# Optimization experiments

Hardware: AMD Instinct MI355X
Metric: run time of the kernel (lower is better)

Reference implementation:

```python
import jax, jax.numpy as jnp
import numpy as np


def setup_inputs() -> dict:
    key = jax.random.key(0)
    k1, k2 = jax.random.split(key)
    B, Te, Td, D = 16, 1024, 1024, 1024
    encoder_outputs = jax.random.normal(k1, (B, Te, D), dtype=jnp.float32)
    decoder_outputs = jax.random.normal(k2, (B, Td, D), dtype=jnp.float32)
    return {"encoder_outputs": encoder_outputs, "decoder_outputs": decoder_outputs}


def reference(encoder_outputs, decoder_outputs):
    # Luong score: [B, Te, Td] = enc @ dec^T
    luong_score = jnp.einsum("bed,btd->bet", encoder_outputs, decoder_outputs)
    # softmax over encoder-time axis (axis=1), matching K.softmax(..., axis=1)
    attn = jax.nn.softmax(luong_score, axis=1)
    # context vector: sum over encoder time of enc * attn -> [B, Td, D]
    # (original materializes [B, Te, Td, D]; this einsum is the same math)
    encoder_vector = jnp.einsum("bed,bet->btd", encoder_outputs, attn)
    return jnp.concatenate([decoder_outputs, encoder_vector], axis=-1)
```

## Files before the change

kernel.cpp:

```cpp
#include <hip/hip_runtime.h>
#include <hip/hip_bf16.h>
#include <stdint.h>

typedef __bf16 bf16x8 __attribute__((ext_vector_type(8)));
typedef float f32x4 __attribute__((ext_vector_type(4)));

#define B_DIM 16
#define TD 1024
#define TE 1024
#define DD 1024

typedef __attribute__((address_space(1))) void as1_void;
typedef __attribute__((address_space(3))) void as3_void;

#define GLL16(gp, lp) \
  __builtin_amdgcn_global_load_lds((as1_void*)(gp), (as3_void*)(lp), 16, 0, 0)

__device__ __forceinline__ uint32_t rne_bf16(float x) {
  uint32_t u = __builtin_bit_cast(uint32_t, x);
  return (u + 0x7FFFu + ((u >> 16) & 1u)) >> 16;
}

__device__ __forceinline__ void split2(float x, uint32_t& hi, uint32_t& lo) {
  uint32_t h = rne_bf16(x);
  float hf = __builtin_bit_cast(float, h << 16);
  hi = h;
  lo = rne_bf16(x - hf);
}

__global__ __launch_bounds__(256)
void p0a_split_dec(const float4* __restrict__ dec4, uint32_t* __restrict__ dhi,
                   uint32_t* __restrict__ dlo) {
  size_t g = (size_t)blockIdx.x * 256 + threadIdx.x;
#pragma unroll
  for (int s = 0; s < 8; ++s, g += 524288) {
    float4 v = dec4[g];
    uint32_t h0, l0, h1, l1, h2, l2, h3, l3;
    split2(v.x, h0, l0);
    split2(v.y, h1, l1);
    split2(v.z, h2, l2);
    split2(v.w, h3, l3);
    *(uint2*)&dhi[g * 2] = make_uint2(h0 | (h1 << 16), h2 | (h3 << 16));
    *(uint2*)&dlo[g * 2] = make_uint2(l0 | (l1 << 16), l2 | (l3 << 16));
  }
}

__global__ __launch_bounds__(256)
void p0b_split_enc(const float* __restrict__ enc, uint32_t* __restrict__ ehi,
                   uint32_t* __restrict__ elo, uint16_t* __restrict__ eT) {
  __shared__ uint16_t TT[64][65];
  const int tid = threadIdx.x;
  const int b = blockIdx.z;
  const int d0 = (blockIdx.x & 15) * 64, e0 = (blockIdx.x >> 4) * 64;
  const float* src = enc + (size_t)b * TE * DD;
#pragma unroll
  for (int s = 0; s < 4; ++s) {
    int c = tid + 256 * s;
    int row = c >> 4, c4 = c & 15;
    float4 v = *(const float4*)(src + (size_t)(e0 + row) * DD + d0 + c4 * 4);
    uint32_t h0, l0, h1, l1, h2, l2, h3, l3;
    split2(v.x, h0, l0);
    split2(v.y, h1, l1);
    split2(v.z, h2, l2);
    split2(v.w, h3, l3);
    size_t o = (((size_t)b * TE + e0 + row) * DD + d0 + c4 * 4) >> 1;
    *(uint2*)&ehi[o] = make_uint2(h0 | (h1 << 16), h2 | (h3 << 16));
    *(uint2*)&elo[o] = make_uint2(l0 | (l1 << 16), l2 | (l3 << 16));
    TT[row][c4 * 4 + 0] = (uint16_t)h0;
    TT[row][c4 * 4 + 1] = (uint16_t)h1;
    TT[row][c4 * 4 + 2] = (uint16_t)h2;
    TT[row][c4 * 4 + 3] = (uint16_t)h3;
  }
  __syncthreads();
#pragma unroll
  for (int s = 0; s < 4; ++s) {
    int c = tid + 256 * s;
    int d = c >> 4, e4 = c & 15;
    uint32_t w0 = (uint32_t)TT[e4 * 4 + 0][d] | ((uint32_t)TT[e4 * 4 + 1][d] << 16);
    uint32_t w1 = (uint32_t)TT[e4 * 4 + 2][d] | ((uint32_t)TT[e4 * 4 + 3][d] << 16);
    *(uint2*)&eT[((size_t)b * DD + d0 + d) * TE + e0 + e4 * 4] = make_uint2(w0, w1);
  }
}

__global__ __launch_bounds__(256, 2)
void k1_scores_v2(const uint16_t* __restrict__ dhi, const uint16_t* __restrict__ dlo,
                  const uint16_t* __restrict__ ehi, const uint16_t* __restrict__ elo,
                  float* __restrict__ out) {
  __shared__ uint32_t AhU[2048], AlU[2048], BhU[2048], BlU[2048];
  const int tid = threadIdx.x;
  const int lane = tid & 63;
  const int wave = tid >> 6;
  const int wm = wave >> 1, wn = wave & 1;
  const int b = blockIdx.z;
  const int t0 = blockIdx.y * 128, e0 = blockIdx.x * 128;

  const int r2 = tid >> 2, c16 = tid & 3;
  const size_t abase = ((size_t)b * TD + t0 + r2) * DD + c16 * 8;
  const size_t bbase = ((size_t)b * TE + e0 + r2) * DD + c16 * 8;

  const int lr = lane & 15, q = lane >> 4;
  int aoff[4], boff[4];
#pragma unroll
  for (int i = 0; i < 4; ++i) {
    aoff[i] = (wm * 64 + i * 16 + lr) * 16 + q * 4;
    boff[i] = (wn * 64 + i * 16 + lr) * 16 + q * 4;
  }

  f32x4 acc[4][4] = {};

  for (int k0 = 0; k0 < DD; k0 += 32) {
    GLL16(dhi + abase + k0, (char*)AhU + tid * 16);
    GLL16(dhi + abase + k0 + 64 * DD, (char*)AhU + tid * 16 + 4096);
    GLL16(dlo + abase + k0, (char*)AlU + tid * 16);
    GLL16(dlo + abase + k0 + 64 * DD, (char*)AlU + tid * 16 + 4096);
    GLL16(ehi + bbase + k0, (char*)BhU + tid * 16);
    GLL16(ehi + bbase + k0 + 64 * DD, (char*)BhU + tid * 16 + 4096);
    GLL16(elo + bbase + k0, (char*)BlU + tid * 16);
    GLL16(elo + bbase + k0 + 64 * DD, (char*)BlU + tid * 16 + 4096);
    __syncthreads();

    bf16x8 ah[4], al[4];
#pragma unroll
    for (int mi = 0; mi < 4; ++mi) {
      ah[mi] = *(const bf16x8*)&AhU[aoff[mi]];
      al[mi] = *(const bf16x8*)&AlU[aoff[mi]];
    }
#pragma unroll
    for (int ni = 0; ni < 4; ++ni) {
      bf16x8 bh = *(const bf16x8*)&BhU[boff[ni]];
      bf16x8 bl = *(const bf16x8*)&BlU[boff[ni]];
#pragma unroll
      for (int mi = 0; mi < 4; ++mi) {
        f32x4 c = acc[mi][ni];
        c = __builtin_amdgcn_mfma_f32_16x16x32_bf16(al[mi], bh, c, 0, 0, 0);
        c = __builtin_amdgcn_mfma_f32_16x16x32_bf16(ah[mi], bl, c, 0, 0, 0);
        c = __builtin_amdgcn_mfma_f32_16x16x32_bf16(ah[mi], bh, c, 0, 0, 0);
        acc[mi][ni] = c;
      }
    }
    __syncthreads();
  }

  float* outb = out + (size_t)b * TD * 2048 + 1024;
  const int tb = t0 + wm * 64 + q * 4;
  const int eb = e0 + wn * 64 + lr;
#pragma unroll
  for (int mi = 0; mi < 4; ++mi)
#pragma unroll
    for (int ni = 0; ni < 4; ++ni)
#pragma unroll
      for (int i = 0; i < 4; ++i)
        outb[(size_t)(tb + mi * 16 + i) * 2048 + (eb + ni * 16)] = acc[mi][ni][i];
}

__global__ __launch_bounds__(256)
void k2_softmax_v2(const float* __restrict__ dec, float* __restrict__ out,
                   uint16_t* __restrict__ P) {
  const int lane = threadIdx.x & 63;
  const int row = blockIdx.x * 4 + (threadIdx.x >> 6);
  const float* Srow = out + (size_t)row * 2048 + 1024;
  float4 v[4];
#pragma unroll
  for (int s = 0; s < 4; ++s) v[s] = *(const float4*)(Srow + lane * 4 + s * 256);
  float m = -1e30f;
#pragma unroll
  for (int s = 0; s < 4; ++s)
    m = fmaxf(m, fmaxf(fmaxf(v[s].x, v[s].y), fmaxf(v[s].z, v[s].w)));
#pragma unroll
  for (int o = 32; o > 0; o >>= 1) m = fmaxf(m, __shfl_xor(m, o));
  float e[16];
  float sum = 0.f;
#pragma unroll
  for (int s = 0; s < 4; ++s) {
    e[4 * s + 0] = __expf(v[s].x - m);
    e[4 * s + 1] = __expf(v[s].y - m);
    e[4 * s + 2] = __expf(v[s].z - m);
    e[4 * s + 3] = __expf(v[s].w - m);
    sum += e[4 * s + 0] + e[4 * s + 1] + e[4 * s + 2] + e[4 * s + 3];
  }
#pragma unroll
  for (int o = 32; o > 0; o >>= 1) sum += __shfl_xor(sum, o);
  const float inv = 1.0f / sum;
  uint32_t* Prow = (uint32_t*)(P + (size_t)row * 1024);
#pragma unroll
  for (int s = 0; s < 4; ++s) {
    uint32_t r0 = rne_bf16(e[4 * s + 0] * inv);
    uint32_t r1 = rne_bf16(e[4 * s + 1] * inv);
    uint32_t r2 = rne_bf16(e[4 * s + 2] * inv);
    uint32_t r3 = rne_bf16(e[4 * s + 3] * inv);
    *(uint2*)&Prow[lane * 2 + s * 128] =
        make_uint2(r0 | (r1 << 16), r2 | (r3 << 16));
  }
  const float4* d4 = (const float4*)(dec + (size_t)row * 1024);
  float4* o4 = (float4*)(out + (size_t)row * 2048);
#pragma unroll
  for (int s = 0; s < 4; ++s) o4[lane + s * 64] = d4[lane + s * 64];
}

__global__ __launch_bounds__(256, 2)
void k3_av_v2(const uint16_t* __restrict__ P, const uint16_t* __restrict__ eT,
              float* __restrict__ out) {
  __shared__ uint32_t AU[2048], BU[2048];
  const int tid = threadIdx.x;
  const int lane = tid & 63, wave = tid >> 6;
  const int wm = wave >> 1, wn = wave & 1;
  const int b = blockIdx.z;
  const int t0 = blockIdx.y * 128, d0 = blockIdx.x * 128;
  const int r2 = tid >> 2, c16 = tid & 3;
  const size_t abase = ((size_t)b * TD + t0 + r2) * TE + c16 * 8;
  const size_t bbase = ((size_t)b * DD + d0 + r2) * TE + c16 * 8;
  const int lr = lane & 15, q = lane >> 4;
  int aoff[4], boff[4];
#pragma unroll
  for (int i = 0; i < 4; ++i) {
    aoff[i] = (wm * 64 + i * 16 + lr) * 16 + q * 4;
    boff[i] = (wn * 64 + i * 16 + lr) * 16 + q * 4;
  }
  f32x4 acc[4][4] = {};

  for (int e0k = 0; e0k < TE; e0k += 32) {
    GLL16(P + abase + e0k, (char*)AU + tid * 16);
    GLL16(P + abase + e0k + 64 * TE, (char*)AU + tid * 16 + 4096);
    GLL16(eT + bbase + e0k, (char*)BU + tid * 16);
    GLL16(eT + bbase + e0k + 64 * TE, (char*)BU + tid * 16 + 4096);
    __syncthreads();

    bf16x8 af[4];
#pragma unroll
    for (int mi = 0; mi < 4; ++mi) af[mi] = *(const bf16x8*)&AU[aoff[mi]];
#pragma unroll
    for (int ni = 0; ni < 4; ++ni) {
      bf16x8 bfr = *(const bf16x8*)&BU[boff[ni]];
#pragma unroll
      for (int mi = 0; mi < 4; ++mi)
        acc[mi][ni] =
            __builtin_amdgcn_mfma_f32_16x16x32_bf16(af[mi], bfr, acc[mi][ni], 0, 0, 0);
    }
    __syncthreads();
  }

  float* outb = out + (size_t)b * TD * 2048 + 1024;
  const int tb = t0 + wm * 64 + q * 4;
  const int db = d0 + wn * 64 + lr;
#pragma unroll
  for (int mi = 0; mi < 4; ++mi)
#pragma unroll
    for (int ni = 0; ni < 4; ++ni)
#pragma unroll
      for (int i = 0; i < 4; ++i)
        outb[(size_t)(tb + mi * 16 + i) * 2048 + (db + ni * 16)] = acc[mi][ni][i];
}

__global__ __launch_bounds__(256, 2)
void k1_scores(const float* __restrict__ dec, const float* __restrict__ enc,
               float* __restrict__ out) {
  __shared__ uint32_t AhU[2048], AlU[2048], BhU[2048], BlU[2048];
  const int tid = threadIdx.x;
  const int lane = tid & 63;
  const int wave = tid >> 6;
  const int wm = wave >> 1, wn = wave & 1;
  const int b = blockIdx.z;
  const int t0 = blockIdx.y * 128, e0 = blockIdx.x * 128;
  const float* A = dec + (size_t)b * TD * DD;
  const float* Bm = enc + (size_t)b * TE * DD;

  const int r = tid >> 3, c4 = tid & 7;
  const float* aptr = A + (size_t)(t0 + r) * DD + c4 * 4;
  const float* bptr = Bm + (size_t)(e0 + r) * DD + c4 * 4;

  const int lr = lane & 15, q = lane >> 4;
  int aoff[4], boff[4];
#pragma unroll
  for (int i = 0; i < 4; ++i) {
    aoff[i] = (wm * 64 + i * 16 + lr) * 16 + q * 4;
    boff[i] = (wn * 64 + i * 16 + lr) * 16 + q * 4;
  }

  f32x4 acc[4][4] = {};

  for (int k0 = 0; k0 < DD; k0 += 32) {
#pragma unroll
    for (int s = 0; s < 4; ++s) {
      const float4 va = *(const float4*)(aptr + (size_t)(32 * s) * DD);
      const float4 vb = *(const float4*)(bptr + (size_t)(32 * s) * DD);
      const int woff = (r + 32 * s) * 16 + c4 * 2;
      {
        uint32_t u0 = __builtin_bit_cast(uint32_t, va.x);
        uint32_t u1 = __builtin_bit_cast(uint32_t, va.y);
        uint32_t u2 = __builtin_bit_cast(uint32_t, va.z);
        uint32_t u3 = __builtin_bit_cast(uint32_t, va.w);
        uint32_t m0 = u0 & 0xFFFF0000u, m1 = u1 & 0xFFFF0000u;
        uint32_t m2 = u2 & 0xFFFF0000u, m3 = u3 & 0xFFFF0000u;
        float l0 = va.x - __builtin_bit_cast(float, m0);
        float l1 = va.y - __builtin_bit_cast(float, m1);
        float l2 = va.z - __builtin_bit_cast(float, m2);
        float l3 = va.w - __builtin_bit_cast(float, m3);
        *(uint2*)&AhU[woff] = make_uint2((m0 >> 16) | m1, (m2 >> 16) | m3);
        *(uint2*)&AlU[woff] = make_uint2(
            (__builtin_bit_cast(uint32_t, l0) >> 16) |
                (__builtin_bit_cast(uint32_t, l1) & 0xFFFF0000u),
            (__builtin_bit_cast(uint32_t, l2) >> 16) |
                (__builtin_bit_cast(uint32_t, l3) & 0xFFFF0000u));
      }
      {
        uint32_t u0 = __builtin_bit_cast(uint32_t, vb.x);
        uint32_t u1 = __builtin_bit_cast(uint32_t, vb.y);
        uint32_t u2 = __builtin_bit_cast(uint32_t, vb.z);
        uint32_t u3 = __builtin_bit_cast(uint32_t, vb.w);
        uint32_t m0 = u0 & 0xFFFF0000u, m1 = u1 & 0xFFFF0000u;
        uint32_t m2 = u2 & 0xFFFF0000u, m3 = u3 & 0xFFFF0000u;
        float l0 = vb.x - __builtin_bit_cast(float, m0);
        float l1 = vb.y - __builtin_bit_cast(float, m1);
        float l2 = vb.z - __builtin_bit_cast(float, m2);
        float l3 = vb.w - __builtin_bit_cast(float, m3);
        *(uint2*)&BhU[woff] = make_uint2((m0 >> 16) | m1, (m2 >> 16) | m3);
        *(uint2*)&BlU[woff] = make_uint2(
            (__builtin_bit_cast(uint32_t, l0) >> 16) |
                (__builtin_bit_cast(uint32_t, l1) & 0xFFFF0000u),
            (__builtin_bit_cast(uint32_t, l2) >> 16) |
                (__builtin_bit_cast(uint32_t, l3) & 0xFFFF0000u));
      }
    }
    __syncthreads();

    bf16x8 ah[4], al[4];
#pragma unroll
    for (int mi = 0; mi < 4; ++mi) {
      ah[mi] = *(const bf16x8*)&AhU[aoff[mi]];
      al[mi] = *(const bf16x8*)&AlU[aoff[mi]];
    }
#pragma unroll
    for (int ni = 0; ni < 4; ++ni) {
      bf16x8 bh = *(const bf16x8*)&BhU[boff[ni]];
      bf16x8 bl = *(const bf16x8*)&BlU[boff[ni]];
#pragma unroll
      for (int mi = 0; mi < 4; ++mi) {
        f32x4 c = acc[mi][ni];
        c = __builtin_amdgcn_mfma_f32_16x16x32_bf16(al[mi], bh, c, 0, 0, 0);
        c = __builtin_amdgcn_mfma_f32_16x16x32_bf16(ah[mi], bl, c, 0, 0, 0);
        c = __builtin_amdgcn_mfma_f32_16x16x32_bf16(ah[mi], bh, c, 0, 0, 0);
        acc[mi][ni] = c;
      }
    }
    __syncthreads();
    aptr += 32;
    bptr += 32;
  }

  float* outb = out + (size_t)b * TD * 2048 + 1024;
  const int tb = t0 + wm * 64 + q * 4;
  const int eb = e0 + wn * 64 + lr;
#pragma unroll
  for (int mi = 0; mi < 4; ++mi)
#pragma unroll
    for (int ni = 0; ni < 4; ++ni)
#pragma unroll
      for (int i = 0; i < 4; ++i)
        outb[(size_t)(tb + mi * 16 + i) * 2048 + (eb + ni * 16)] = acc[mi][ni][i];
}

__global__ __launch_bounds__(256)
void k2_softmax(float* out) {
  const int lane = threadIdx.x & 63;
  const int row = blockIdx.x * 4 + (threadIdx.x >> 6);
  float* Srow = out + (size_t)row * 2048 + 1024;
  float4 v[4];
#pragma unroll
  for (int s = 0; s < 4; ++s) v[s] = *(const float4*)(Srow + lane * 4 + s * 256);
  float m = -1e30f;
#pragma unroll
  for (int s = 0; s < 4; ++s)
    m = fmaxf(m, fmaxf(fmaxf(v[s].x, v[s].y), fmaxf(v[s].z, v[s].w)));
#pragma unroll
  for (int o = 32; o > 0; o >>= 1) m = fmaxf(m, __shfl_xor(m, o));
  float e[16];
  float sum = 0.f;
#pragma unroll
  for (int s = 0; s < 4; ++s) {
    e[4 * s + 0] = __expf(v[s].x - m);
    e[4 * s + 1] = __expf(v[s].y - m);
    e[4 * s + 2] = __expf(v[s].z - m);
    e[4 * s + 3] = __expf(v[s].w - m);
    sum += e[4 * s + 0] + e[4 * s + 1] + e[4 * s + 2] + e[4 * s + 3];
  }
#pragma unroll
  for (int o = 32; o > 0; o >>= 1) sum += __shfl_xor(sum, o);
  const float inv = 1.0f / sum;
  uint32_t* Prow = (uint32_t*)(out + (size_t)row * 2048);
#pragma unroll
  for (int s = 0; s < 4; ++s) {
    uint32_t r0 = rne_bf16(e[4 * s + 0] * inv);
    uint32_t r1 = rne_bf16(e[4 * s + 1] * inv);
    uint32_t r2 = rne_bf16(e[4 * s + 2] * inv);
    uint32_t r3 = rne_bf16(e[4 * s + 3] * inv);
    *(uint2*)&Prow[lane * 2 + s * 128] =
        make_uint2(r0 | (r1 << 16), r2 | (r3 << 16));
  }
}

__global__ __launch_bounds__(256, 2)
void k3_av(const float* __restrict__ enc, float* __restrict__ out) {
  __shared__ uint32_t AU[2048];
  __shared__ uint32_t BtU[128 * 20];
  const int tid = threadIdx.x;
  const int lane = tid & 63, wave = tid >> 6;
  const int wm = wave >> 1, wn = wave & 1;
  const int b = blockIdx.z;
  const int t0 = blockIdx.y * 128, d0 = blockIdx.x * 128;
  const float* V = enc + (size_t)b * TE * DD;
  const uint16_t* Pb = (const uint16_t*)(out + (size_t)b * TD * 2048);
  const int lr = lane & 15, q = lane >> 4;
  int aoff[4], boff[4];
#pragma unroll
  for (int i = 0; i < 4; ++i) {
    aoff[i] = (wm * 64 + i * 16 + lr) * 16 + q * 4;
    boff[i] = (wn * 64 + i * 16 + lr) * 20 + q * 4;
  }
  const int dB = tid & 127;
  f32x4 acc[4][4] = {};

  for (int e0k = 0; e0k < TE; e0k += 32) {
#pragma unroll
    for (int s = 0; s < 2; ++s) {
      int c = tid + 256 * s;
      int rc = c >> 2, cc = c & 3;
      uint4 va = *(const uint4*)(Pb + (size_t)(t0 + rc) * 4096 + e0k + cc * 8);
      *(uint4*)&AU[c * 4] = va;
    }
#pragma unroll
    for (int s = 0; s < 4; ++s) {
      int eg = (tid >> 7) + 2 * s;
      const float* src = V + (size_t)(e0k + eg * 4) * DD + d0 + dB;
      float x0 = src[0], x1 = src[DD], x2 = src[2 * DD], x3 = src[3 * DD];
      uint32_t r0 = rne_bf16(x0), r1 = rne_bf16(x1);
      uint32_t r2 = rne_bf16(x2), r3 = rne_bf16(x3);
      *(uint2*)&BtU[dB * 20 + eg * 2] =
          make_uint2(r0 | (r1 << 16), r2 | (r3 << 16));
    }
    __syncthreads();

    bf16x8 af[4];
#pragma unroll
    for (int mi = 0; mi < 4; ++mi) af[mi] = *(const bf16x8*)&AU[aoff[mi]];
#pragma unroll
    for (int ni = 0; ni < 4; ++ni) {
      bf16x8 bfr = *(const bf16x8*)&BtU[boff[ni]];
#pragma unroll
      for (int mi = 0; mi < 4; ++mi)
        acc[mi][ni] =
            __builtin_amdgcn_mfma_f32_16x16x32_bf16(af[mi], bfr, acc[mi][ni], 0, 0, 0);
    }
    __syncthreads();
  }

  float* outb = out + (size_t)b * TD * 2048 + 1024;
  const int tb = t0 + wm * 64 + q * 4;
  const int db = d0 + wn * 64 + lr;
#pragma unroll
  for (int mi = 0; mi < 4; ++mi)
#pragma unroll
    for (int ni = 0; ni < 4; ++ni)
#pragma unroll
      for (int i = 0; i < 4; ++i)
        outb[(size_t)(tb + mi * 16 + i) * 2048 + (db + ni * 16)] = acc[mi][ni][i];
}

__global__ __launch_bounds__(256)
void k4_copydec(const float4* __restrict__ dec4, float4* __restrict__ out4) {
  size_t g = (size_t)blockIdx.x * 512 + threadIdx.x;
#pragma unroll
  for (int s = 0; s < 2; ++s, g += 256) {
    size_t row = g >> 8, col = g & 255;
    out4[row * 512 + col] = dec4[g];
  }
}

extern "C" void kernel_launch(void* const* d_in, const int* in_sizes, int n_in,
                              void* d_out, int out_size, void* d_ws, size_t ws_size,
                              hipStream_t stream) {
  const float* enc = (const float*)d_in[0];
  const float* dec = (const float*)d_in[1];
  float* out = (float*)d_out;

  const size_t M32 = 32ull << 20;
  if (d_ws != nullptr && ws_size >= 5 * M32) {
    char* ws = (char*)d_ws;
    uint16_t* dhi = (uint16_t*)(ws);
    uint16_t* dlo = (uint16_t*)(ws + M32);
    uint16_t* ehi = (uint16_t*)(ws + 2 * M32);
    uint16_t* elo = (uint16_t*)(ws + 3 * M32);
    uint16_t* eT = (uint16_t*)(ws + 4 * M32);
    uint16_t* P = dhi;

    hipLaunchKernelGGL(p0a_split_dec, dim3(2048), dim3(256), 0, stream,
                       (const float4*)dec, (uint32_t*)dhi, (uint32_t*)dlo);
    hipLaunchKernelGGL(p0b_split_enc, dim3(256, 1, 16), dim3(256), 0, stream,
                       enc, (uint32_t*)ehi, (uint32_t*)elo, eT);
    hipLaunchKernelGGL(k1_scores_v2, dim3(8, 8, 16), dim3(256), 0, stream,
                       dhi, dlo, ehi, elo, out);
    hipLaunchKernelGGL(k2_softmax_v2, dim3(4096), dim3(256), 0, stream, dec, out, P);
    hipLaunchKernelGGL(k3_av_v2, dim3(8, 8, 16), dim3(256), 0, stream, P, eT, out);
  } else {
    hipLaunchKernelGGL(k1_scores, dim3(8, 8, 16), dim3(256), 0, stream, dec, enc, out);
    hipLaunchKernelGGL(k2_softmax, dim3(4096), dim3(256), 0, stream, out);
    hipLaunchKernelGGL(k3_av, dim3(8, 8, 16), dim3(256), 0, stream, enc, out);
    hipLaunchKernelGGL(k4_copydec, dim3(8192), dim3(256), 0, stream,
                       (const float4*)dec, (float4*)out);
  }
}
```

Before: 463.0 us.

## Replace GEMM kernels with 256x256 tiled double-buffered LDS-swizzled pipelined GEMM

Replaces the 128x128 score and attention-value GEMM kernels with a single templated 256x256-tile kernel using 512 threads and 128KB of dynamic LDS. It double-buffers global-to-LDS loads with explicit vmcnt waits, XOR-swizzles LDS to avoid bank conflicts, and raises wave priority around MFMA blocks. The three-way bf16 split product is expressed as three K-segments concatenated in one loop, and a block-index swizzle is meant to improve L2 locality. This targets load latency and LDS bandwidth costs in exchange for one block per CU and only 256 blocks, which is fewer than before.

```diff
diff --git a/kernel.cpp b/kernel.cpp
--- a/kernel.cpp
+++ b/kernel.cpp
@@ -15,6 +15,19 @@
 
 #define GLL16(gp, lp) \
   __builtin_amdgcn_global_load_lds((as1_void*)(gp), (as3_void*)(lp), 16, 0, 0)
+
+#define SB __builtin_amdgcn_sched_barrier(0)
+#define BAR()                      \
+  do {                             \
+    SB;                            \
+    __builtin_amdgcn_s_barrier();  \
+    SB;                            \
+  } while (0)
+#define VMW2()                                       \
+  do {                                               \
+    asm volatile("s_waitcnt vmcnt(2)" ::: "memory"); \
+    SB;                                              \
+  } while (0)
 
 __device__ __forceinline__ uint32_t rne_bf16(float x) {
   uint32_t u = __builtin_bit_cast(uint32_t, x);
@@ -82,75 +95,134 @@
   }
 }
 
-__global__ __launch_bounds__(256, 2)
-void k1_scores_v2(const uint16_t* __restrict__ dhi, const uint16_t* __restrict__ dlo,
-                  const uint16_t* __restrict__ ehi, const uint16_t* __restrict__ elo,
-                  float* __restrict__ out) {
-  __shared__ uint32_t AhU[2048], AlU[2048], BhU[2048], BlU[2048];
+template <int NSEG>
+__global__ __launch_bounds__(512, 2)
+void k_gemm256(const uint16_t* __restrict__ a0, const uint16_t* __restrict__ a1,
+               const uint16_t* __restrict__ a2, const uint16_t* __restrict__ b0,
+               const uint16_t* __restrict__ b1, const uint16_t* __restrict__ b2,
+               float* __restrict__ out) {
+  extern __shared__ char lds[];
   const int tid = threadIdx.x;
-  const int lane = tid & 63;
-  const int wave = tid >> 6;
-  const int wm = wave >> 1, wn = wave & 1;
-  const int b = blockIdx.z;
-  const int t0 = blockIdx.y * 128, e0 = blockIdx.x * 128;
-
-  const int r2 = tid >> 2, c16 = tid & 3;
-  const size_t abase = ((size_t)b * TD + t0 + r2) * DD + c16 * 8;
-  const size_t bbase = ((size_t)b * TE + e0 + r2) * DD + c16 * 8;
-
+  const int lane = tid & 63, wave = tid >> 6;
+  const int wr = wave >> 2, wc = wave & 3;
   const int lr = lane & 15, q = lane >> 4;
-  int aoff[4], boff[4];
-#pragma unroll
-  for (int i = 0; i < 4; ++i) {
-    aoff[i] = (wm * 64 + i * 16 + lr) * 16 + q * 4;
-    boff[i] = (wn * 64 + i * 16 + lr) * 16 + q * 4;
-  }
-
-  f32x4 acc[4][4] = {};
-
-  for (int k0 = 0; k0 < DD; k0 += 32) {
-    GLL16(dhi + abase + k0, (char*)AhU + tid * 16);
-    GLL16(dhi + abase + k0 + 64 * DD, (char*)AhU + tid * 16 + 4096);
-    GLL16(dlo + abase + k0, (char*)AlU + tid * 16);
-    GLL16(dlo + abase + k0 + 64 * DD, (char*)AlU + tid * 16 + 4096);
-    GLL16(ehi + bbase + k0, (char*)BhU + tid * 16);
-    GLL16(ehi + bbase + k0 + 64 * DD, (char*)BhU + tid * 16 + 4096);
-    GLL16(elo + bbase + k0, (char*)BlU + tid * 16);
-    GLL16(elo + bbase + k0 + 64 * DD, (char*)BlU + tid * 16 + 4096);
-    __syncthreads();
-
-    bf16x8 ah[4], al[4];
-#pragma unroll
-    for (int mi = 0; mi < 4; ++mi) {
-      ah[mi] = *(const bf16x8*)&AhU[aoff[mi]];
-      al[mi] = *(const bf16x8*)&AlU[aoff[mi]];
-    }
-#pragma unroll
-    for (int ni = 0; ni < 4; ++ni) {
-      bf16x8 bh = *(const bf16x8*)&BhU[boff[ni]];
-      bf16x8 bl = *(const bf16x8*)&BlU[boff[ni]];
-#pragma unroll
-      for (int mi = 0; mi < 4; ++mi) {
-        f32x4 c = acc[mi][ni];
-        c = __builtin_amdgcn_mfma_f32_16x16x32_bf16(al[mi], bh, c, 0, 0, 0);
-        c = __builtin_amdgcn_mfma_f32_16x16x32_bf16(ah[mi], bl, c, 0, 0, 0);
-        c = __builtin_amdgcn_mfma_f32_16x16x32_bf16(ah[mi], bh, c, 0, 0, 0);
-        acc[mi][ni] = c;
-      }
-    }
-    __syncthreads();
-  }
-
-  float* outb = out + (size_t)b * TD * 2048 + 1024;
-  const int tb = t0 + wm * 64 + q * 4;
-  const int eb = e0 + wn * 64 + lr;
-#pragma unroll
-  for (int mi = 0; mi < 4; ++mi)
+
+  const int id = blockIdx.x;
+  const int swz = (id & 7) * 32 + (id >> 3);
+  const int b = swz >> 4, mblk = (swz >> 2) & 3, nblk = swz & 3;
+  const size_t bOff = (size_t)b << 20;
+  const uint16_t* As[3] = {a0 + bOff, a1 + bOff, a2 + bOff};
+  const uint16_t* Bs[3] = {b0 + bOff, b1 + bOff, b2 + bOff};
+  const int mrow0 = mblk * 256, nrow0 = nblk * 256;
+  constexpr int T = NSEG * 16;
+
+  f32x4 acc[8][4] = {};
+  bf16x8 a[8], bA[2], bB[2];
+
+  auto STAGE = [&](int op, int half, int tau, int buf) {
+    int seg, klt;
+    if constexpr (NSEG == 3) {
+      seg = tau >> 4;
+      klt = tau & 15;
+    } else {
+      seg = 0;
+      klt = tau;
+    }
+    const uint16_t* base = (op == 0 ? As[seg] : Bs[seg]) +
+                           (size_t)((op == 0 ? mrow0 : nrow0) + half * 128) * 1024 +
+                           klt * 64;
+    char* dst = lds + (((buf * 2 + op) * 2 + half) << 14);
+#pragma unroll
+    for (int j = 0; j < 2; ++j) {
+      int chunk = j * 512 + tid;
+      int row = chunk >> 3;
+      int k8 = ((chunk & 7) ^ (row & 7)) << 3;
+      GLL16(base + (size_t)row * 1024 + k8, dst + chunk * 16);
+    }
+  };
+
+  auto LDA = [&](int kk, int buf) {
+    const char* src = lds + (((buf * 2 + 0) * 2 + wr) << 14);
+#pragma unroll
+    for (int mi = 0; mi < 8; ++mi) {
+      int rl = mi * 16 + lr;
+      int col = (kk * 64 + q * 16) ^ ((rl & 7) << 4);
+      a[mi] = *(const bf16x8*)(src + rl * 128 + col);
+    }
+  };
+  auto LDB = [&](int kk, int nbase, bf16x8* bb, int buf) {
+    const char* src = lds + (((buf * 2 + 1) * 2 + (wc >> 1)) << 14);
+#pragma unroll
+    for (int u = 0; u < 2; ++u) {
+      int rl = (wc & 1) * 64 + (nbase + u) * 16 + lr;
+      int col = (kk * 64 + q * 16) ^ ((rl & 7) << 4);
+      bb[u] = *(const bf16x8*)(src + rl * 128 + col);
+    }
+  };
+  auto MFMAQ = [&](bf16x8* bb, int npair) {
+#pragma unroll
+    for (int u = 0; u < 2; ++u)
+#pragma unroll
+      for (int mi = 0; mi < 8; ++mi)
+        acc[mi][npair * 2 + u] = __builtin_amdgcn_mfma_f32_16x16x32_bf16(
+            a[mi], bb[u], acc[mi][npair * 2 + u], 0, 0, 0);
+  };
+
+  STAGE(0, 0, 0, 0);
+  STAGE(1, 0, 0, 0);
+  STAGE(0, 1, 0, 0);
+  STAGE(1, 1, 0, 0);
+  STAGE(0, 0, 1, 1);
+  VMW2();
+  BAR();
+
+  for (int t = 0; t < T; ++t) {
+    const int cur = t & 1, nxt = cur ^ 1;
+    const int t1 = (t + 1 < T) ? t + 1 : 0;
+    const int t2 = (t + 2 < T) ? t + 2 : t + 2 - T;
+    LDA(0, cur);
+    LDB(0, 0, bA, cur);
+    STAGE(1, 0, t1, nxt);
+    BAR();
+    __builtin_amdgcn_s_setprio(1);
+    MFMAQ(bA, 0);
+    __builtin_amdgcn_s_setprio(0);
+    BAR();
+    LDB(0, 2, bB, cur);
+    STAGE(0, 1, t1, nxt);
+    BAR();
+    __builtin_amdgcn_s_setprio(1);
+    MFMAQ(bB, 1);
+    __builtin_amdgcn_s_setprio(0);
+    BAR();
+    LDA(1, cur);
+    LDB(1, 2, bB, cur);
+    STAGE(1, 1, t1, nxt);
+    BAR();
+    __builtin_amdgcn_s_setprio(1);
+    MFMAQ(bB, 1);
+    __builtin_amdgcn_s_setprio(0);
+    BAR();
+    LDB(1, 0, bA, cur);
+    STAGE(0, 0, t2, cur);
+    VMW2();
+    BAR();
+    __builtin_amdgcn_s_setprio(1);
+    MFMAQ(bA, 0);
+    __builtin_amdgcn_s_setprio(0);
+    BAR();
+  }
+
+  float* outp = out + (size_t)b * TD * 2048 + 1024;
+  const int m0 = mrow0 + wr * 128 + q * 4;
+  const int n0 = nrow0 + wc * 64 + lr;
+#pragma unroll
+  for (int mi = 0; mi < 8; ++mi)
 #pragma unroll
     for (int ni = 0; ni < 4; ++ni)
 #pragma unroll
       for (int i = 0; i < 4; ++i)
-        outb[(size_t)(tb + mi * 16 + i) * 2048 + (eb + ni * 16)] = acc[mi][ni][i];
+        outp[(size_t)(m0 + mi * 16 + i) * 2048 + (n0 + ni * 16)] = acc[mi][ni][i];
 }
 
 __global__ __launch_bounds__(256)
@@ -195,60 +267,6 @@
   float4* o4 = (float4*)(out + (size_t)row * 2048);
 #pragma unroll
   for (int s = 0; s < 4; ++s) o4[lane + s * 64] = d4[lane + s * 64];
-}
-
-__global__ __launch_bounds__(256, 2)
-void k3_av_v2(const uint16_t* __restrict__ P, const uint16_t* __restrict__ eT,
-              float* __restrict__ out) {
-  __shared__ uint32_t AU[2048], BU[2048];
-  const int tid = threadIdx.x;
-  const int lane = tid & 63, wave = tid >> 6;
-  const int wm = wave >> 1, wn = wave & 1;
-  const int b = blockIdx.z;
-  const int t0 = blockIdx.y * 128, d0 = blockIdx.x * 128;
-  const int r2 = tid >> 2, c16 = tid & 3;
-  const size_t abase = ((size_t)b * TD + t0 + r2) * TE + c16 * 8;
-  const size_t bbase = ((size_t)b * DD + d0 + r2) * TE + c16 * 8;
-  const int lr = lane & 15, q = lane >> 4;
-  int aoff[4], boff[4];
-#pragma unroll
-  for (int i = 0; i < 4; ++i) {
-    aoff[i] = (wm * 64 + i * 16 + lr) * 16 + q * 4;
-    boff[i] = (wn * 64 + i * 16 + lr) * 16 + q * 4;
-  }
-  f32x4 acc[4][4] = {};
-
-  for (int e0k = 0; e0k < TE; e0k += 32) {
-    GLL16(P + abase + e0k, (char*)AU + tid * 16);
-    GLL16(P + abase + e0k + 64 * TE, (char*)AU + tid * 16 + 4096);
-    GLL16(eT + bbase + e0k, (char*)BU + tid * 16);
-    GLL16(eT + bbase + e0k + 64 * TE, (char*)BU + tid * 16 + 4096);
-    __syncthreads();
-
-    bf16x8 af[4];
-#pragma unroll
-    for (int mi = 0; mi < 4; ++mi) af[mi] = *(const bf16x8*)&AU[aoff[mi]];
-#pragma unroll
-    for (int ni = 0; ni < 4; ++ni) {
-      bf16x8 bfr = *(const bf16x8*)&BU[boff[ni]];
-#pragma unroll
-      for (int mi = 0; mi < 4; ++mi)
-        acc[mi][ni] =
-            __builtin_amdgcn_mfma_f32_16x16x32_bf16(af[mi], bfr, acc[mi][ni], 0, 0, 0);
-    }
-    __syncthreads();
-  }
-
-  float* outb = out + (size_t)b * TD * 2048 + 1024;
-  const int tb = t0 + wm * 64 + q * 4;
-  const int db = d0 + wn * 64 + lr;
-#pragma unroll
-  for (int mi = 0; mi < 4; ++mi)
-#pragma unroll
-    for (int ni = 0; ni < 4; ++ni)
-#pragma unroll
-      for (int i = 0; i < 4; ++i)
-        outb[(size_t)(tb + mi * 16 + i) * 2048 + (db + ni * 16)] = acc[mi][ni][i];
 }
 
 __global__ __launch_bounds__(256, 2)
@@ -483,7 +501,18 @@
   float* out = (float*)d_out;
 
   const size_t M32 = 32ull << 20;
-  if (d_ws != nullptr && ws_size >= 5 * M32) {
+  bool fast = (d_ws != nullptr) && (ws_size >= 5 * M32);
+  if (fast) {
+    hipError_t e1 = hipFuncSetAttribute(
+        (const void*)k_gemm256<3>, hipFuncAttributeMaxDynamicSharedMemorySize,
+        131072);
+    hipError_t e2 = hipFuncSetAttribute(
+        (const void*)k_gemm256<1>, hipFuncAttributeMaxDynamicSharedMemorySize,
+        131072);
+    if (e1 != hipSuccess || e2 != hipSuccess) fast = false;
+  }
+
+  if (fast) {
     char* ws = (char*)d_ws;
     uint16_t* dhi = (uint16_t*)(ws);
     uint16_t* dlo = (uint16_t*)(ws + M32);
@@ -496,10 +525,11 @@
                        (const float4*)dec, (uint32_t*)dhi, (uint32_t*)dlo);
     hipLaunchKernelGGL(p0b_split_enc, dim3(256, 1, 16), dim3(256), 0, stream,
                        enc, (uint32_t*)ehi, (uint32_t*)elo, eT);
-    hipLaunchKernelGGL(k1_scores_v2, dim3(8, 8, 16), dim3(256), 0, stream,
-                       dhi, dlo, ehi, elo, out);
+    hipLaunchKernelGGL(k_gemm256<3>, dim3(256), dim3(512), 131072, stream,
+                       dhi, dhi, dlo, ehi, elo, ehi, out);
     hipLaunchKernelGGL(k2_softmax_v2, dim3(4096), dim3(256), 0, stream, dec, out, P);
-    hipLaunchKernelGGL(k3_av_v2, dim3(8, 8, 16), dim3(256), 0, stream, P, eT, out);
+    hipLaunchKernelGGL(k_gemm256<1>, dim3(256), dim3(512), 131072, stream,
+                       P, P, P, eT, eT, eT, out);
   } else {
     hipLaunchKernelGGL(k1_scores, dim3(8, 8, 16), dim3(256), 0, stream, dec, enc, out);
     hipLaunchKernelGGL(k2_softmax, dim3(4096), dim3(256), 0, stream, out);
```

Result: faster. 416.0 us (-10.1%).
